# Kernel optimization log

Hardware: AMD Instinct MI355X
Metric: run time of the kernel (lower is better)

## Reference

```python
import jax, jax.numpy as jnp
import numpy as np

N_HEADS = 16
POOL_WIDTH = 3


def setup_inputs() -> dict:
    key = jax.random.key(0)
    ks = jax.random.split(key, 6)
    B, S, D = 4, 1024, 1024
    x = jax.random.normal(ks[0], (B, S, D), dtype=jnp.float32)
    W_q = jax.random.normal(ks[1], (D, D), dtype=jnp.float32) * 0.02
    W_k = jax.random.normal(ks[2], (D, D), dtype=jnp.float32) * 0.02
    W_v = jax.random.normal(ks[3], (D, D), dtype=jnp.float32) * 0.02
    W_o = jax.random.normal(ks[4], (D, D), dtype=jnp.float32) * 0.02
    freq_raw = jnp.zeros((D,), dtype=jnp.float32)
    pool_raw = jnp.array([0.25, 1.0, 0.25], dtype=jnp.float32)
    return {"x": x, "W_q": W_q, "W_k": W_k, "W_v": W_v, "W_o": W_o,
            "freq_raw": freq_raw, "pool_raw": pool_raw}


def _spectral_attention(x, W_q, W_k, W_v, W_o, freq_raw, pool_raw):
    B, S, D = x.shape
    H = N_HEADS
    hd = D // H
    pw = POOL_WIDTH
    pad = pw // 2

    # projections (torch Linear: y = x @ W.T)
    Q = x @ W_q.T
    K = x @ W_k.T
    V = x @ W_v.T

    # monotone non-increasing freq weights: reverse cumsum of softplus
    fw = jnp.flip(jnp.cumsum(jnp.flip(jax.nn.softplus(freq_raw))))
    # symmetric, positive pool weights
    pwts = jax.nn.softplus((pool_raw + jnp.flip(pool_raw)) * 0.5)

    Qh = (Q * fw).reshape(B, S, H, hd).transpose(0, 2, 1, 3)  # [B,H,S,hd]
    K_pad = jnp.pad(K, ((0, 0), (0, 0), (pad, pad)))          # [B,S,D+2*pad]

    scores = jnp.zeros((B, H, S, S), dtype=x.dtype)
    for i in range(pw):  # small fixed loop over pool offsets
        K_shift = jax.lax.dynamic_slice_in_dim(K_pad, i, D, axis=2)
        Kh = K_shift.reshape(B, S, H, hd).transpose(0, 2, 1, 3)
        scores = scores + pwts[i] * jnp.einsum('bhqd,bhkd->bhqk', Qh, Kh)
    scores = scores / np.sqrt(hd).astype(x.dtype)

    causal = jnp.tril(jnp.ones((S, S), dtype=bool))
    scores = jnp.where(causal, scores, jnp.finfo(scores.dtype).min)
    attn = jax.nn.softmax(scores, axis=-1)

    Vh = V.reshape(B, S, H, hd).transpose(0, 2, 1, 3)
    out = jnp.einsum('bhqk,bhkd->bhqd', attn, Vh)
    out = out.transpose(0, 2, 1, 3).reshape(B, S, D)
    return out @ W_o.T


def reference(x, W_q, W_k, W_v, W_o, freq_raw, pool_raw):
    return _spectral_attention(x, W_q, W_k, W_v, W_o, freq_raw, pool_raw)
```

## Files before the change

kernel.cpp:

```cpp
#include <hip/hip_runtime.h>

typedef __attribute__((ext_vector_type(8))) short short8;
typedef __attribute__((ext_vector_type(4))) float float4v;
typedef __attribute__((ext_vector_type(4))) float floatx4;
typedef __attribute__((ext_vector_type(4))) unsigned short ushort4v;

#define DEV static __device__ __forceinline__
#define MFMA __builtin_amdgcn_mfma_f32_16x16x32_bf16

DEV unsigned short f2bf(float f){
  unsigned u = __builtin_bit_cast(unsigned, f);
  unsigned r = u + 0x7FFFu + ((u >> 16) & 1u);
  return (unsigned short)(r >> 16);
}
DEV float bf2f(unsigned short h){
  unsigned u = ((unsigned)h) << 16;
  return __builtin_bit_cast(float, u);
}
DEV float softplus_f(float x){
  if (x > 20.f) return x;
  return log1pf(expf(x));
}

DEV void gload16(const void* g, void* l){
  __builtin_amdgcn_global_load_lds(
      (const __attribute__((address_space(1))) unsigned int*)g,
      (__attribute__((address_space(3))) unsigned int*)l, 16, 0, 0);
}

__global__ __launch_bounds__(256) void k_prep(
    const float* __restrict__ freq_raw, const float* __restrict__ pool_raw,
    const float* __restrict__ x,
    const float* __restrict__ Wq, const float* __restrict__ Wk,
    const float* __restrict__ Wv, const float* __restrict__ Wo,
    unsigned short* __restrict__ wq_h, unsigned short* __restrict__ wq_l,
    unsigned short* __restrict__ wk_h, unsigned short* __restrict__ wk_l,
    unsigned short* __restrict__ wv_b, unsigned short* __restrict__ wo_b,
    unsigned short* __restrict__ xh, unsigned short* __restrict__ xl){
  int g = blockIdx.x;
  int tid = threadIdx.x;
  if (g < 1024){
    __shared__ float red[256];
    int n = g;
    float s = 0.f;
    for (int j = tid; j < 1024; j += 256)
      if (j >= n) s += softplus_f(freq_raw[j]);
    red[tid] = s;
    __syncthreads();
    for (int off = 128; off > 0; off >>= 1){
      if (tid < off) red[tid] += red[tid + off];
      __syncthreads();
    }
    float f = red[0] * 0.125f;
    float p0 = softplus_f((pool_raw[0] + pool_raw[2]) * 0.5f);
    float p1 = softplus_f(pool_raw[1]);
    float p2 = p0;

    int k4 = tid << 2;
    int o = n * 1024 + k4;
    float4v q4 = *(const float4v*)(Wq + o);
    float4v k0v = *(const float4v*)(Wk + o);
    float4v km = {0.f,0.f,0.f,0.f}, kp = {0.f,0.f,0.f,0.f};
    if (n > 0)    km = *(const float4v*)(Wk + o - 1024);
    if (n < 1023) kp = *(const float4v*)(Wk + o + 1024);
    float4v v4 = *(const float4v*)(Wv + o);
    float4v o4 = *(const float4v*)(Wo + o);
    ushort4v qh, ql, kh, kl, vb, ob;
    for (int j = 0; j < 4; j++){
      float wq_ = f * q4[j];
      unsigned short h = f2bf(wq_);
      qh[j] = h; ql[j] = f2bf(wq_ - bf2f(h));
      float wk_ = p0 * km[j] + p1 * k0v[j] + p2 * kp[j];
      h = f2bf(wk_);
      kh[j] = h; kl[j] = f2bf(wk_ - bf2f(h));
      vb[j] = f2bf(v4[j]);
      ob[j] = f2bf(o4[j]);
    }
    *(ushort4v*)(wq_h + o) = qh; *(ushort4v*)(wq_l + o) = ql;
    *(ushort4v*)(wk_h + o) = kh; *(ushort4v*)(wk_l + o) = kl;
    *(ushort4v*)(wv_b + o) = vb; *(ushort4v*)(wo_b + o) = ob;
  } else {
    int idx = (g - 1024) * 256 + tid;
    int o = idx * 4;
    float4v v = *(const float4v*)(x + o);
    ushort4v h4, l4;
    for (int j = 0; j < 4; j++){
      unsigned short h = f2bf(v[j]);
      h4[j] = h; l4[j] = f2bf(v[j] - bf2f(h));
    }
    *(ushort4v*)(xh + o) = h4;
    *(ushort4v*)(xl + o) = l4;
  }
}

__global__ __launch_bounds__(256) void k_qkv(
    const unsigned short* __restrict__ Ah, const unsigned short* __restrict__ Al,
    const unsigned short* __restrict__ Bqh, const unsigned short* __restrict__ Bql,
    const unsigned short* __restrict__ Bkh, const unsigned short* __restrict__ Bkl,
    const unsigned short* __restrict__ Bvh,
    unsigned short* __restrict__ qh_o, unsigned short* __restrict__ ql_o,
    unsigned short* __restrict__ kh_o, unsigned short* __restrict__ kl_o,
    unsigned short* __restrict__ vt_o){
  __shared__ unsigned short lds[2][18432];
  int tid = threadIdx.x;
  int w = tid >> 6, l = tid & 63, lg = l >> 4, lr = l & 15;
  int wr = w >> 1, wc = w & 1;
  int g = blockIdx.x;
  int mblk = (g & 7) * 4 + ((g >> 3) & 3);
  int nblk = g >> 5;
  int m0 = mblk * 128, n0 = nblk * 64;

  auto stage = [&](int kt, int bufi){
    unsigned short* buf = lds[bufi];
    for (int rep = 0; rep < 2; rep++){
      int idx = rep * 256 + tid;
      int r = idx >> 2, c = idx & 3;
      int cs = (c ^ ((r >> 1) & 3)) * 8;
      int srcA = (m0 + r) * 1024 + kt + cs;
      unsigned short* dst = buf + rep * 2048 + w * 512;
      gload16(Ah + srcA, dst);
      gload16(Al + srcA, dst + 4096);
    }
    {
      int r = tid >> 2, c = tid & 3;
      int cs = (c ^ ((r >> 1) & 3)) * 8;
      int srcB = (n0 + r) * 1024 + kt + cs;
      unsigned short* dst = buf + 8192 + w * 512;
      gload16(Bqh + srcB, dst);
      gload16(Bql + srcB, dst + 2048);
      gload16(Bkh + srcB, dst + 4096);
      gload16(Bkl + srcB, dst + 6144);
      gload16(Bvh + srcB, dst + 8192);
    }
  };

  floatx4 aq[4][2] = {}, ak[4][2] = {}, av[4][2] = {};
  stage(0, 0);
  __syncthreads();
  int cur = 0;
  for (int kt = 0; kt < 1024; kt += 32){
    if (kt + 32 < 1024) stage(kt + 32, cur ^ 1);
    const unsigned short* buf = lds[cur];
    short8 a_h[4], a_l[4], bq_h[2], bq_l[2], bk_h[2], bk_l[2], bv_h[2];
    #pragma unroll
    for (int ms = 0; ms < 4; ms++){
      int r = wr * 64 + ms * 16 + lr;
      int off = r * 32 + ((lg ^ ((r >> 1) & 3)) * 8);
      a_h[ms] = *(const short8*)(buf + off);
      a_l[ms] = *(const short8*)(buf + 4096 + off);
    }
    #pragma unroll
    for (int ns = 0; ns < 2; ns++){
      int r = wc * 32 + ns * 16 + lr;
      int off = r * 32 + ((lg ^ ((r >> 1) & 3)) * 8);
      bq_h[ns] = *(const short8*)(buf + 8192 + off);
      bq_l[ns] = *(const short8*)(buf + 10240 + off);
      bk_h[ns] = *(const short8*)(buf + 12288 + off);
      bk_l[ns] = *(const short8*)(buf + 14336 + off);
      bv_h[ns] = *(const short8*)(buf + 16384 + off);
    }
    #pragma unroll
    for (int ms = 0; ms < 4; ms++)
      #pragma unroll
      for (int ns = 0; ns < 2; ns++){
        aq[ms][ns] = MFMA(a_h[ms], bq_h[ns], aq[ms][ns], 0, 0, 0);
        aq[ms][ns] = MFMA(a_h[ms], bq_l[ns], aq[ms][ns], 0, 0, 0);
        aq[ms][ns] = MFMA(a_l[ms], bq_h[ns], aq[ms][ns], 0, 0, 0);
        ak[ms][ns] = MFMA(a_h[ms], bk_h[ns], ak[ms][ns], 0, 0, 0);
        ak[ms][ns] = MFMA(a_h[ms], bk_l[ns], ak[ms][ns], 0, 0, 0);
        ak[ms][ns] = MFMA(a_l[ms], bk_h[ns], ak[ms][ns], 0, 0, 0);
        av[ms][ns] = MFMA(a_h[ms], bv_h[ns], av[ms][ns], 0, 0, 0);
      }
    __syncthreads();
    cur ^= 1;
  }
  for (int ms = 0; ms < 4; ms++)
    for (int ns = 0; ns < 2; ns++){
      int mrow = m0 + wr * 64 + ms * 16 + lg * 4;
      int ncol = n0 + wc * 32 + ns * 16 + lr;
      for (int rr = 0; rr < 4; rr++){
        int o = (mrow + rr) * 1024 + ncol;
        float v = aq[ms][ns][rr];
        unsigned short hh = f2bf(v);
        qh_o[o] = hh; ql_o[o] = f2bf(v - bf2f(hh));
        v = ak[ms][ns][rr];
        hh = f2bf(v);
        kh_o[o] = hh; kl_o[o] = f2bf(v - bf2f(hh));
      }
      int tb = m0 + wr * 64;
      int bq = tb >> 10, sg = (tb >> 6) & 15;
      int P0 = ((ms >> 1) << 5) | (lg << 3) | ((ms & 1) << 2);
      ushort4v v4;
      for (int rr = 0; rr < 4; rr++) v4[rr] = f2bf(av[ms][ns][rr]);
      *(ushort4v*)(vt_o + (ncol * 4 + bq) * 1024 + sg * 64 + P0) = v4;
    }
}

template<int OUT>
__global__ __launch_bounds__(256) void k_gemm(
    const unsigned short* __restrict__ Ah, const unsigned short* __restrict__ Bh,
    void* __restrict__ out0, int M, int N, int K){
  constexpr int BUFN = 6144;
  __shared__ unsigned short lds[3 * BUFN];
  int tid = threadIdx.x;
  int w = tid >> 6, l = tid & 63, lg = l >> 4, lr = l & 15;
  int wr = w >> 1, wc = w & 1;
  int n0 = blockIdx.x * 128, m0 = blockIdx.y * 64;

  auto stage = [&](int kt, int bufi){
    unsigned short* buf = lds + bufi * BUFN;
    { int r = tid >> 2, c = tid & 3;
      int src = (m0 + r) * K + kt + (c ^ ((r >> 1) & 3)) * 8;
      gload16(Ah + src, buf + w * 512); }
    for (int rep = 0; rep < 2; rep++){
      int idx = rep * 256 + tid;
      int r = idx >> 2, c = idx & 3;
      int src = (n0 + r) * K + kt + (c ^ ((r >> 1) & 3)) * 8;
      gload16(Bh + src, buf + 2048 + rep * 2048 + w * 512);
    }
  };

  floatx4 acc[2][4] = {};
  int nT = K >> 5;
  stage(0, 0);
  stage(32, 1);
  for (int t = 0; t < nT; ++t){
    if (t == nT - 1) asm volatile("s_waitcnt vmcnt(0)" ::: "memory");
    else             asm volatile("s_waitcnt vmcnt(3)" ::: "memory");
    __builtin_amdgcn_sched_barrier(0);
    __builtin_amdgcn_s_barrier();
    __builtin_amdgcn_sched_barrier(0);
    if (t + 2 < nT) stage((t + 2) * 32, (t + 2) % 3);

    const unsigned short* buf = lds + (t % 3) * BUFN;
    short8 a_h[2], b_h[4];
    #pragma unroll
    for (int ms = 0; ms < 2; ms++){
      int r = wr * 32 + ms * 16 + lr;
      int off = r * 32 + ((lg ^ ((r >> 1) & 3)) * 8);
      a_h[ms] = *(const short8*)(buf + off);
    }
    #pragma unroll
    for (int ns = 0; ns < 4; ns++){
      int r = wc * 64 + ns * 16 + lr;
      int off = r * 32 + ((lg ^ ((r >> 1) & 3)) * 8);
      b_h[ns] = *(const short8*)(buf + 2048 + off);
    }
    #pragma unroll
    for (int ms = 0; ms < 2; ms++)
      #pragma unroll
      for (int ns = 0; ns < 4; ns++)
        acc[ms][ns] = MFMA(a_h[ms], b_h[ns], acc[ms][ns], 0, 0, 0);
  }
  for (int ms = 0; ms < 2; ms++)
    for (int ns = 0; ns < 4; ns++){
      int mrow = m0 + wr * 32 + ms * 16 + lg * 4;
      int ncol = n0 + wc * 64 + ns * 16 + lr;
      for (int rr = 0; rr < 4; rr++){
        float v = acc[ms][ns][rr];
        int o = (mrow + rr) * N + ncol;
        if constexpr (OUT == 2) ((float*)out0)[o] = v;
        else                    ((unsigned short*)out0)[o] = f2bf(v);
      }
    }
}

__global__ __launch_bounds__(256) void k_attn(
    const unsigned short* __restrict__ Qh, const unsigned short* __restrict__ Ql,
    const unsigned short* __restrict__ Kh, const unsigned short* __restrict__ Kl,
    const unsigned short* __restrict__ Vt, unsigned short* __restrict__ Ob){
  __shared__ unsigned short s_k[2][12288];
  int tid = threadIdx.x;
  int w = tid >> 6, l = tid & 63, lg = l >> 4, lr = l & 15;
  int gx = blockIdx.x;
  int bh = gx & 63, qt = 15 - (gx >> 6);
  int b = bh >> 4, h = bh & 15;
  int q0 = qt * 64;
  int qs = q0 + w * 16;
  int rowb = b * 1024;

  auto stage = [&](int kt, int bufi){
    int k0 = kt * 64;
    unsigned short* buf = s_k[bufi];
    for (int rep = 0; rep < 2; rep++){
      int idx = rep * 256 + tid;
      int r = idx >> 3, c = idx & 7;
      int cs = c ^ (r & 7);
      int srcK = (rowb + k0 + r) * 1024 + h * 64 + cs * 8;
      int srcV = ((h * 64 + r) * 4 + b) * 1024 + k0 + cs * 8;
      unsigned short* dst = buf + rep * 2048 + w * 512;
      gload16(Kh + srcK, dst);
      gload16(Kl + srcK, dst + 4096);
      gload16(Vt + srcV, dst + 8192);
    }
  };

  short8 fqh[2], fql[2];
  for (int ds = 0; ds < 2; ds++){
    int off = (rowb + qs + lr) * 1024 + h * 64 + ds * 32 + lg * 8;
    fqh[ds] = *(const short8*)(Qh + off);
    fql[ds] = *(const short8*)(Ql + off);
  }

  floatx4 oT[4] = {};
  float m_r = -__builtin_inff(), l_r = 0.f;

  int ntile = qt + 1;
  stage(0, 0);
  __syncthreads();
  int cur = 0;
  for (int kt = 0; kt < ntile; kt++){
    int k0 = kt * 64;
    if (kt + 1 < ntile) stage(kt + 1, cur ^ 1);
    const unsigned short* kb = s_k[cur];

    floatx4 sc[4] = {};
    __builtin_amdgcn_s_setprio(1);
    for (int ds = 0; ds < 2; ds++)
      for (int s = 0; s < 4; s++){
        int r = s * 16 + lr;
        int off = r * 64 + (((ds * 4 + lg) ^ (r & 7)) * 8);
        short8 kh_f = *(const short8*)(kb + off);
        short8 kl_f = *(const short8*)(kb + 4096 + off);
        sc[s] = MFMA(kh_f, fqh[ds], sc[s], 0, 0, 0);
        sc[s] = MFMA(kl_f, fqh[ds], sc[s], 0, 0, 0);
        sc[s] = MFMA(kh_f, fql[ds], sc[s], 0, 0, 0);
      }
    __builtin_amdgcn_s_setprio(0);

    if (kt == ntile - 1){
      #pragma unroll
      for (int s = 0; s < 4; s++)
        #pragma unroll
        for (int rr = 0; rr < 4; rr++)
          if (k0 + s * 16 + 4 * lg + rr > qs + lr) sc[s][rr] = -__builtin_inff();
    }

    float mx = sc[0][0];
    #pragma unroll
    for (int s = 0; s < 4; s++)
      #pragma unroll
      for (int rr = 0; rr < 4; rr++) mx = fmaxf(mx, sc[s][rr]);
    mx = fmaxf(mx, __shfl_xor(mx, 16));
    mx = fmaxf(mx, __shfl_xor(mx, 32));
    float mn = fmaxf(m_r, mx);
    float fac = __expf(m_r - mn);
    m_r = mn;
    float ps = 0.f;
    #pragma unroll
    for (int s = 0; s < 4; s++)
      #pragma unroll
      for (int rr = 0; rr < 4; rr++){
        float p = __expf(sc[s][rr] - mn);
        sc[s][rr] = p;
        ps += p;
      }
    ps += __shfl_xor(ps, 16);
    ps += __shfl_xor(ps, 32);
    l_r = l_r * fac + ps;
    #pragma unroll
    for (int dsb = 0; dsb < 4; dsb++) oT[dsb] *= fac;

    __builtin_amdgcn_s_setprio(1);
    #pragma unroll
    for (int kk = 0; kk < 2; kk++){
      short8 pb;
      #pragma unroll
      for (int j = 0; j < 8; j++)
        pb[j] = (short)f2bf(sc[2 * kk + (j >> 2)][j & 3]);
      #pragma unroll
      for (int dsb = 0; dsb < 4; dsb++){
        int rv = dsb * 16 + lr;
        int offv = rv * 64 + (((kk * 4 + lg) ^ (rv & 7)) * 8);
        short8 vb = *(const short8*)(kb + 8192 + offv);
        oT[dsb] = MFMA(vb, pb, oT[dsb], 0, 0, 0);
      }
    }
    __builtin_amdgcn_s_setprio(0);
    __syncthreads();
    cur ^= 1;
  }

  float inv = 1.f / l_r;
  int base = (rowb + qs + lr) * 1024 + h * 64;
  #pragma unroll
  for (int dsb = 0; dsb < 4; dsb++){
    ushort4v o4;
    #pragma unroll
    for (int rr = 0; rr < 4; rr++) o4[rr] = f2bf(oT[dsb][rr] * inv);
    *(ushort4v*)(Ob + base + dsb * 16 + 4 * lg) = o4;
  }
}

extern "C" void kernel_launch(void* const* d_in, const int* in_sizes, int n_in,
                              void* d_out, int out_size, void* d_ws, size_t ws_size,
                              hipStream_t stream){
  const float* x  = (const float*)d_in[0];
  const float* Wq = (const float*)d_in[1];
  const float* Wk = (const float*)d_in[2];
  const float* Wv = (const float*)d_in[3];
  const float* Wo = (const float*)d_in[4];
  const float* fr = (const float*)d_in[5];
  const float* pr = (const float*)d_in[6];

  char* ws = (char*)d_ws;
  size_t off = 0;
  auto alloc = [&](size_t bytes) -> char* {
    char* p = ws + off;
    off += (bytes + 255) & ~(size_t)255;
    return p;
  };
  const size_t WB = (size_t)1024 * 1024 * 2;
  unsigned short* wq_h = (unsigned short*)alloc(WB);
  unsigned short* wq_l = (unsigned short*)alloc(WB);
  unsigned short* wk_h = (unsigned short*)alloc(WB);
  unsigned short* wk_l = (unsigned short*)alloc(WB);
  unsigned short* wv_b = (unsigned short*)alloc(WB);
  unsigned short* wo_b = (unsigned short*)alloc(WB);
  const size_t XB = (size_t)4096 * 1024 * 2;
  unsigned short* x_h = (unsigned short*)alloc(XB);
  unsigned short* x_l = (unsigned short*)alloc(XB);
  unsigned short* q_h = (unsigned short*)alloc(XB);
  unsigned short* q_l = (unsigned short*)alloc(XB);
  unsigned short* k_h = (unsigned short*)alloc(XB);
  unsigned short* k_l = (unsigned short*)alloc(XB);
  unsigned short* vt  = (unsigned short*)alloc(XB);
  unsigned short* o_b = x_l;

  k_prep<<<5120, 256, 0, stream>>>(fr, pr, x, Wq, Wk, Wv, Wo,
                                   wq_h, wq_l, wk_h, wk_l, wv_b, wo_b,
                                   x_h, x_l);
  k_qkv<<<512, 256, 0, stream>>>(x_h, x_l, wq_h, wq_l, wk_h, wk_l, wv_b,
                                 q_h, q_l, k_h, k_l, vt);
  k_attn<<<1024, 256, 0, stream>>>(q_h, q_l, k_h, k_l, vt, o_b);
  dim3 ggo(8, 64);
  k_gemm<2><<<ggo, 256, 0, stream>>>(o_b, wo_b, d_out, 4096, 1024, 1024);
}
```

Before: 118.7 us.

## Process two 64-row query tiles per attention block to reuse staged K/V

```diff
diff --git a/kernel.cpp b/kernel.cpp
--- a/kernel.cpp
+++ b/kernel.cpp
@@ -273,11 +273,11 @@
   int tid = threadIdx.x;
   int w = tid >> 6, l = tid & 63, lg = l >> 4, lr = l & 15;
   int gx = blockIdx.x;
-  int bh = gx & 63, qt = 15 - (gx >> 6);
+  int bh = gx & 63, qt = 7 - (gx >> 6);
   int b = bh >> 4, h = bh & 15;
-  int q0 = qt * 64;
-  int qs = q0 + w * 16;
+  int q0 = qt * 128;
   int rowb = b * 1024;
+  int qb[2] = { q0 + w * 16, q0 + 64 + w * 16 };
 
   auto stage = [&](int kt, int bufi){
     int k0 = kt * 64;
@@ -295,17 +295,20 @@
     }
   };
 
-  short8 fqh[2], fql[2];
-  for (int ds = 0; ds < 2; ds++){
-    int off = (rowb + qs + lr) * 1024 + h * 64 + ds * 32 + lg * 8;
-    fqh[ds] = *(const short8*)(Qh + off);
-    fql[ds] = *(const short8*)(Ql + off);
-  }
-
-  floatx4 oT[4] = {};
-  float m_r = -__builtin_inff(), l_r = 0.f;
-
-  int ntile = qt + 1;
+  short8 fqh[2][2], fql[2][2];
+  for (int qm = 0; qm < 2; qm++)
+    for (int ds = 0; ds < 2; ds++){
+      int off = (rowb + qb[qm] + lr) * 1024 + h * 64 + ds * 32 + lg * 8;
+      fqh[qm][ds] = *(const short8*)(Qh + off);
+      fql[qm][ds] = *(const short8*)(Ql + off);
+    }
+
+  floatx4 oT[2][4] = {};
+  float m_[2], l_[2];
+  m_[0] = m_[1] = -__builtin_inff();
+  l_[0] = l_[1] = 0.f;
+
+  int ntile = 2 * qt + 2;
   stage(0, 0);
   __syncthreads();
   int cur = 0;
@@ -314,66 +317,80 @@
     if (kt + 1 < ntile) stage(kt + 1, cur ^ 1);
     const unsigned short* kb = s_k[cur];
 
-    floatx4 sc[4] = {};
-    __builtin_amdgcn_s_setprio(1);
-    for (int ds = 0; ds < 2; ds++)
-      for (int s = 0; s < 4; s++){
-        int r = s * 16 + lr;
-        int off = r * 64 + (((ds * 4 + lg) ^ (r & 7)) * 8);
-        short8 kh_f = *(const short8*)(kb + off);
-        short8 kl_f = *(const short8*)(kb + 4096 + off);
-        sc[s] = MFMA(kh_f, fqh[ds], sc[s], 0, 0, 0);
-        sc[s] = MFMA(kl_f, fqh[ds], sc[s], 0, 0, 0);
-        sc[s] = MFMA(kh_f, fql[ds], sc[s], 0, 0, 0);
-      }
-    __builtin_amdgcn_s_setprio(0);
-
-    if (kt == ntile - 1){
+    floatx4 sc[2][4];
+    bool act0 = (kt < ntile - 1);
+    #pragma unroll
+    for (int qm = 0; qm < 2; qm++){
+      if (qm == 0 && !act0) continue;
+      #pragma unroll
+      for (int s = 0; s < 4; s++) sc[qm][s] = floatx4{0.f,0.f,0.f,0.f};
+      __builtin_amdgcn_s_setprio(1);
+      for (int ds = 0; ds < 2; ds++)
+        for (int s = 0; s < 4; s++){
+          int r = s * 16 + lr;
+          int off = r * 64 + (((ds * 4 + lg) ^ (r & 7)) * 8);
+          short8 kh_f = *(const short8*)(kb + off);
+          short8 kl_f = *(const short8*)(kb + 4096 + off);
+          sc[qm][s] = MFMA(kh_f, fqh[qm][ds], sc[qm][s], 0, 0, 0);
+          sc[qm][s] = MFMA(kl_f, fqh[qm][ds], sc[qm][s], 0, 0, 0);
+          sc[qm][s] = MFMA(kh_f, fql[qm][ds], sc[qm][s], 0, 0, 0);
+        }
+      __builtin_amdgcn_s_setprio(0);
+
+      bool diag = (qm == 0) ? (kt == ntile - 2) : (kt == ntile - 1);
+      if (diag){
+        int q = qb[qm] + lr;
+        #pragma unroll
+        for (int s = 0; s < 4; s++)
+          #pragma unroll
+          for (int rr = 0; rr < 4; rr++)
+            if (k0 + s * 16 + 4 * lg + rr > q) sc[qm][s][rr] = -__builtin_inff();
+      }
+
+      float mx = sc[qm][0][0];
       #pragma unroll
       for (int s = 0; s < 4; s++)
         #pragma unroll
-        for (int rr = 0; rr < 4; rr++)
-          if (k0 + s * 16 + 4 * lg + rr > qs + lr) sc[s][rr] = -__builtin_inff();
-    }
-
-    float mx = sc[0][0];
-    #pragma unroll
-    for (int s = 0; s < 4; s++)
-      #pragma unroll
-      for (int rr = 0; rr < 4; rr++) mx = fmaxf(mx, sc[s][rr]);
-    mx = fmaxf(mx, __shfl_xor(mx, 16));
-    mx = fmaxf(mx, __shfl_xor(mx, 32));
-    float mn = fmaxf(m_r, mx);
-    float fac = __expf(m_r - mn);
-    m_r = mn;
-    float ps = 0.f;
-    #pragma unroll
-    for (int s = 0; s < 4; s++)
-      #pragma unroll
-      for (int rr = 0; rr < 4; rr++){
-        float p = __expf(sc[s][rr] - mn);
-        sc[s][rr] = p;
-        ps += p;
-      }
-    ps += __shfl_xor(ps, 16);
-    ps += __shfl_xor(ps, 32);
-    l_r = l_r * fac + ps;
-    #pragma unroll
-    for (int dsb = 0; dsb < 4; dsb++) oT[dsb] *= fac;
+        for (int rr = 0; rr < 4; rr++) mx = fmaxf(mx, sc[qm][s][rr]);
+      mx = fmaxf(mx, __shfl_xor(mx, 16));
+      mx = fmaxf(mx, __shfl_xor(mx, 32));
+      float mn = fmaxf(m_[qm], mx);
+      float fac = __expf(m_[qm] - mn);
+      m_[qm] = mn;
+      float ps = 0.f;
+      #pragma unroll
+      for (int s = 0; s < 4; s++)
+        #pragma unroll
+        for (int rr = 0; rr < 4; rr++){
+          float p = __expf(sc[qm][s][rr] - mn);
+          sc[qm][s][rr] = p;
+          ps += p;
+        }
+      ps += __shfl_xor(ps, 16);
+      ps += __shfl_xor(ps, 32);
+      l_[qm] = l_[qm] * fac + ps;
+      #pragma unroll
+      for (int dsb = 0; dsb < 4; dsb++) oT[qm][dsb] *= fac;
+    }
 
     __builtin_amdgcn_s_setprio(1);
     #pragma unroll
     for (int kk = 0; kk < 2; kk++){
-      short8 pb;
-      #pragma unroll
-      for (int j = 0; j < 8; j++)
-        pb[j] = (short)f2bf(sc[2 * kk + (j >> 2)][j & 3]);
+      short8 pb[2];
+      #pragma unroll
+      for (int qm = 0; qm < 2; qm++){
+        if (qm == 0 && !act0) continue;
+        #pragma unroll
+        for (int j = 0; j < 8; j++)
+          pb[qm][j] = (short)f2bf(sc[qm][2 * kk + (j >> 2)][j & 3]);
+      }
       #pragma unroll
       for (int dsb = 0; dsb < 4; dsb++){
         int rv = dsb * 16 + lr;
         int offv = rv * 64 + (((kk * 4 + lg) ^ (rv & 7)) * 8);
         short8 vb = *(const short8*)(kb + 8192 + offv);
-        oT[dsb] = MFMA(vb, pb, oT[dsb], 0, 0, 0);
+        if (act0) oT[0][dsb] = MFMA(vb, pb[0], oT[0][dsb], 0, 0, 0);
+        oT[1][dsb] = MFMA(vb, pb[1], oT[1][dsb], 0, 0, 0);
       }
     }
     __builtin_amdgcn_s_setprio(0);
@@ -381,14 +398,17 @@
     cur ^= 1;
   }
 
-  float inv = 1.f / l_r;
-  int base = (rowb + qs + lr) * 1024 + h * 64;
   #pragma unroll
-  for (int dsb = 0; dsb < 4; dsb++){
-    ushort4v o4;
-    #pragma unroll
-    for (int rr = 0; rr < 4; rr++) o4[rr] = f2bf(oT[dsb][rr] * inv);
-    *(ushort4v*)(Ob + base + dsb * 16 + 4 * lg) = o4;
+  for (int qm = 0; qm < 2; qm++){
+    float inv = 1.f / l_[qm];
+    int base = (rowb + qb[qm] + lr) * 1024 + h * 64;
+    #pragma unroll
+    for (int dsb = 0; dsb < 4; dsb++){
+      ushort4v o4;
+      #pragma unroll
+      for (int rr = 0; rr < 4; rr++) o4[rr] = f2bf(oT[qm][dsb][rr] * inv);
+      *(ushort4v*)(Ob + base + dsb * 16 + 4 * lg) = o4;
+    }
   }
 }
 
@@ -432,7 +452,7 @@
                                    x_h, x_l);
   k_qkv<<<512, 256, 0, stream>>>(x_h, x_l, wq_h, wq_l, wk_h, wk_l, wv_b,
                                  q_h, q_l, k_h, k_l, vt);
-  k_attn<<<1024, 256, 0, stream>>>(q_h, q_l, k_h, k_l, vt, o_b);
+  k_attn<<<512, 256, 0, stream>>>(q_h, q_l, k_h, k_l, vt, o_b);
   dim3 ggo(8, 64);
   k_gemm<2><<<ggo, 256, 0, stream>>>(o_b, wo_b, d_out, 4096, 1024, 1024);
 }
```

Result: slower. 132.3 us (+11.4%).
